# Performance work log

Measured on AMD Instinct MI355X. Metric: run time of the kernel, lower is better.

## Reference

```python
import jax, jax.numpy as jnp
import numpy as np
from jax import lax

B, T, EPROJS, DUNITS, ATT_DIM = 32, 2048, 1024, 1024, 512
ACONV_CHANS, ACONV_FILTS = 10, 100
KSIZE = 2 * ACONV_FILTS + 1  # 201
SCALING = 2.0


def setup_inputs() -> dict:
    key = jax.random.key(0)
    ks = jax.random.split(key, 16)
    lengths = jax.random.randint(ks[1], (B,), T // 2, T + 1, dtype=jnp.int32)
    # normalized uniform initial attention over valid frames (as in module's init branch)
    mask = jnp.arange(T)[None, :] < lengths[:, None]
    att_prev = mask.astype(jnp.float32) / lengths[:, None].astype(jnp.float32)
    s_e = 1.0 / np.sqrt(EPROJS)
    s_d = 1.0 / np.sqrt(DUNITS)
    s_a = 1.0 / np.sqrt(ATT_DIM)
    s_c = 1.0 / np.sqrt(ACONV_CHANS)
    return {
        "enc_hs_pad": jax.random.normal(ks[0], (B, T, EPROJS), jnp.float32),
        "enc_hs_len": lengths,
        "dec_z": jax.random.normal(ks[2], (B, DUNITS), jnp.float32),
        "att_prev": att_prev,
        "att_h": jax.random.normal(ks[3], (B, ATT_DIM), jnp.float32) * 0.1,
        "att_c": jax.random.normal(ks[4], (B, ATT_DIM), jnp.float32) * 0.1,
        "W_enc": jax.random.uniform(ks[5], (EPROJS, ATT_DIM), jnp.float32, -s_e, s_e),
        "b_enc": jax.random.uniform(ks[6], (ATT_DIM,), jnp.float32, -s_e, s_e),
        "W_dec": jax.random.uniform(ks[7], (DUNITS, ATT_DIM), jnp.float32, -s_d, s_d),
        "W_conv": jax.random.uniform(ks[8], (ACONV_CHANS, 1, KSIZE), jnp.float32, -0.1, 0.1),
        "W_ih": jax.random.uniform(ks[9], (4 * ATT_DIM, ACONV_CHANS), jnp.float32, -s_a, s_a),
        "W_hh": jax.random.uniform(ks[10], (4 * ATT_DIM, ATT_DIM), jnp.float32, -s_a, s_a),
        "W_g": jax.random.uniform(ks[11], (ATT_DIM, 1), jnp.float32, -s_a, s_a),
        "b_g": jax.random.uniform(ks[12], (1,), jnp.float32, -s_a, s_a),
    }


def reference(enc_hs_pad, enc_hs_len, dec_z, att_prev, att_h, att_c,
              W_enc, b_enc, W_dec, W_conv, W_ih, W_hh, W_g, b_g):
    # pre_compute_enc_h = mlp_enc(enc_h): (B, T, A)
    pre_enc = jnp.einsum("bte,ea->bta", enc_hs_pad, W_enc) + b_enc

    # location conv over previous attention: (B,1,T) -> (B,C,T)
    conv = lax.conv_general_dilated(
        att_prev[:, None, :], W_conv,
        window_strides=(1,), padding=[(ACONV_FILTS, ACONV_FILTS)],
        dimension_numbers=("NCH", "OIH", "NCH"))
    # relu + global max-pool over T -> (B, C)
    conv_feat = jnp.max(jax.nn.relu(conv), axis=2)

    # LSTMCell (no bias), PyTorch gate order i, f, g, o
    gates = conv_feat @ W_ih.T + att_h @ W_hh.T  # (B, 4A)
    i, f, g, o = jnp.split(gates, 4, axis=1)
    c_new = jax.nn.sigmoid(f) * att_c + jax.nn.sigmoid(i) * jnp.tanh(g)
    h_new = jax.nn.sigmoid(o) * jnp.tanh(c_new)

    dec_t = dec_z @ W_dec  # (B, A)
    # scoring: gvec(tanh(att_h + pre_enc + dec)) -> (B, T)
    e = (jnp.tanh(h_new[:, None, :] + pre_enc + dec_t[:, None, :]) @ W_g)[..., 0] + b_g[0]

    pad_mask = jnp.arange(e.shape[1])[None, :] >= enc_hs_len[:, None]
    e = jnp.where(pad_mask, -jnp.inf, e)
    w = jax.nn.softmax(SCALING * e, axis=1)  # (B, T)

    c = jnp.einsum("bt,bte->be", w, enc_hs_pad)  # (B, EPROJS)
    return c, w, h_new, c_new
```

## Files before the change

kernel.cpp:

```cpp
#include <hip/hip_runtime.h>
#include <hip/hip_bf16.h>
#include <cstddef>

#define BB      32
#define TT_ALL  2048
#define EPROJS  1024
#define DUNITS  1024
#define ATT     512
#define CH      10
#define KS      201
#define FILT    100

#define OFF_C   0
#define OFF_W   (BB*EPROJS)
#define OFF_H   (OFF_W + BB*TT_ALL)
#define OFF_CN  (OFF_H + BB*ATT)

#define WS_CF    0
#define WS_V     512
#define WS_E     16896
#define WS_WF    82432
#define WS_WT    147968
#define WS_PART  (WS_WT + 262144)
#define WS_GP    (WS_PART + 262144)
#define WS_DP    (WS_GP + 131072)

typedef __attribute__((ext_vector_type(8))) short short8;
typedef __attribute__((ext_vector_type(4))) float f32x4;

__device__ __forceinline__ float sigm(float x) { return 1.f / (1.f + expf(-x)); }
__device__ __forceinline__ unsigned short f2bf(float f) {
  unsigned u = __float_as_uint(f);
  return (unsigned short)((u + 0x7FFFu + ((u >> 16) & 1u)) >> 16);
}
__device__ __forceinline__ ushort2 f2bf2(float a, float b) {
  __hip_bfloat162 h = __float22bfloat162_rn(float2{a, b});
  return *reinterpret_cast<ushort2*>(&h);
}

__global__ __launch_bounds__(256) void k_wprep(const float* __restrict__ W,
                                               unsigned short* __restrict__ WT) {
  const int et = blockIdx.x >> 4;
  const int at = blockIdx.x & 15;
  const int e0 = et * 32, a0 = at * 32;
  __shared__ float st[32][36];
  const int tid = threadIdx.x;
  {
    const int r = tid >> 3, q = tid & 7;
    const float4 v4 = *reinterpret_cast<const float4*>(&W[(size_t)(e0 + r) * ATT + a0 + q * 4]);
    st[r][q * 4 + 0] = v4.x; st[r][q * 4 + 1] = v4.y;
    st[r][q * 4 + 2] = v4.z; st[r][q * 4 + 3] = v4.w;
  }
  __syncthreads();
  {
    const int a = tid >> 3, q = tid & 7;
    ushort4 h;
    h.x = f2bf(st[q * 4 + 0][a]); h.y = f2bf(st[q * 4 + 1][a]);
    h.z = f2bf(st[q * 4 + 2][a]); h.w = f2bf(st[q * 4 + 3][a]);
    *reinterpret_cast<ushort4*>(&WT[(size_t)(a0 + a) * EPROJS + e0 + q * 4]) = h;
  }
}

__global__ __launch_bounds__(256) void k_conv(const float* __restrict__ att_prev,
                                              const float* __restrict__ W_conv,
                                              float* __restrict__ conv_feat) {
  const int b  = blockIdx.x / CH;
  const int ch = blockIdx.x % CH;
  __shared__ float sprev[TT_ALL + 2 * FILT];
  __shared__ float sw[KS];
  __shared__ float red[4];
  const int tid = threadIdx.x;
  for (int i = tid; i < TT_ALL + 2 * FILT; i += 256) {
    int t = i - FILT;
    sprev[i] = (t >= 0 && t < TT_ALL) ? att_prev[b * TT_ALL + t] : 0.f;
  }
  for (int i = tid; i < KS; i += 256) sw[i] = W_conv[ch * KS + i];
  __syncthreads();
  float m = 0.f;
  for (int t = tid; t < TT_ALL; t += 256) {
    float s = 0.f;
    for (int k = 0; k < KS; ++k) s = fmaf(sprev[t + k], sw[k], s);
    m = fmaxf(m, s);
  }
  for (int off = 32; off; off >>= 1) m = fmaxf(m, __shfl_xor(m, off, 64));
  if ((tid & 63) == 0) red[tid >> 6] = m;
  __syncthreads();
  if (tid == 0)
    conv_feat[b * CH + ch] = fmaxf(fmaxf(red[0], red[1]), fmaxf(red[2], red[3]));
}

__global__ __launch_bounds__(256) void k_gates(const float* __restrict__ att_h,
                                               const float* __restrict__ W_hh,
                                               float* __restrict__ gp) {
  const int jt = blockIdx.x >> 1;
  const int sp = blockIdx.x & 1;
  const int j0 = jt * 64;
  const int k0 = sp * 256;
  const int tid = threadIdx.x;
  const int al = tid & 63, bg = tid >> 6;
  __shared__ float sW[64][65];
  __shared__ float sH[32][64];
  float acc[8];
#pragma unroll
  for (int i = 0; i < 8; ++i) acc[i] = 0.f;
  for (int kc = 0; kc < 256; kc += 64) {
    __syncthreads();
#pragma unroll
    for (int i = 0; i < 4; ++i) {
      const int f = tid + i * 256;
      const int r = f >> 4, q = f & 15;
      const float4 w4 = *reinterpret_cast<const float4*>(
          &W_hh[(size_t)(j0 + r) * ATT + k0 + kc + q * 4]);
      sW[r][q * 4 + 0] = w4.x; sW[r][q * 4 + 1] = w4.y;
      sW[r][q * 4 + 2] = w4.z; sW[r][q * 4 + 3] = w4.w;
    }
#pragma unroll
    for (int i = 0; i < 2; ++i) {
      const int g = tid + i * 256;
      const int r = g >> 4, q = g & 15;
      *reinterpret_cast<float4*>(&sH[r][q * 4]) = *reinterpret_cast<const float4*>(
          &att_h[(size_t)r * ATT + k0 + kc + q * 4]);
    }
    __syncthreads();
#pragma unroll 16
    for (int k = 0; k < 64; ++k) {
      const float w = sW[al][k];
#pragma unroll
      for (int bb = 0; bb < 8; ++bb)
        acc[bb] = fmaf(w, sH[bg * 8 + bb][k], acc[bb]);
    }
  }
#pragma unroll
  for (int bb = 0; bb < 8; ++bb)
    gp[((size_t)(sp * 32 + bg * 8 + bb)) * (4 * ATT) + j0 + al] = acc[bb];
}

__global__ __launch_bounds__(256) void k_dec(const float* __restrict__ dec_z,
                                             const float* __restrict__ W_dec,
                                             float* __restrict__ dp) {
  const int at = blockIdx.x >> 1;
  const int sp = blockIdx.x & 1;
  const int a0 = at * 64;
  const int d0 = sp * 512;
  const int tid = threadIdx.x;
  const int al = tid & 63, bg = tid >> 6;
  __shared__ float sW[64][64];
  __shared__ float sZ[32][64];
  float acc[8];
#pragma unroll
  for (int i = 0; i < 8; ++i) acc[i] = 0.f;
  for (int dc = 0; dc < 512; dc += 64) {
    __syncthreads();
#pragma unroll
    for (int i = 0; i < 4; ++i) {
      const int f = tid + i * 256;
      const int r = f >> 4, q = f & 15;
      *reinterpret_cast<float4*>(&sW[r][q * 4]) = *reinterpret_cast<const float4*>(
          &W_dec[(size_t)(d0 + dc + r) * ATT + a0 + q * 4]);
    }
#pragma unroll
    for (int i = 0; i < 2; ++i) {
      const int g = tid + i * 256;
      const int r = g >> 4, q = g & 15;
      *reinterpret_cast<float4*>(&sZ[r][q * 4]) = *reinterpret_cast<const float4*>(
          &dec_z[(size_t)r * DUNITS + d0 + dc + q * 4]);
    }
    __syncthreads();
#pragma unroll 16
    for (int d = 0; d < 64; ++d) {
      const float w = sW[d][al];
#pragma unroll
      for (int bb = 0; bb < 8; ++bb)
        acc[bb] = fmaf(sZ[bg * 8 + bb][d], w, acc[bb]);
    }
  }
#pragma unroll
  for (int bb = 0; bb < 8; ++bb)
    dp[((size_t)(sp * 32 + bg * 8 + bb)) * ATT + a0 + al] = acc[bb];
}

__global__ __launch_bounds__(256) void k_lstm_v(const float* __restrict__ gp,
                                                const float* __restrict__ dp,
                                                const float* __restrict__ conv_feat,
                                                const float* __restrict__ W_ih,
                                                const float* __restrict__ att_c,
                                                float* __restrict__ v,
                                                float* __restrict__ out) {
  const int b = blockIdx.x, tid = threadIdx.x;
  __shared__ float scf[CH];
  if (tid < CH) scf[tid] = conv_feat[b * CH + tid];
  __syncthreads();
  for (int a = tid; a < ATT; a += 256) {
    float g4[4];
#pragma unroll
    for (int q = 0; q < 4; ++q) {
      const int j = q * ATT + a;
      float g = gp[(size_t)b * (4 * ATT) + j] + gp[(size_t)(32 + b) * (4 * ATT) + j];
#pragma unroll
      for (int c = 0; c < CH; ++c) g = fmaf(scf[c], W_ih[(size_t)j * CH + c], g);
      g4[q] = g;
    }
    const float ig = sigm(g4[0]);
    const float fg = sigm(g4[1]);
    const float gg = tanhf(g4[2]);
    const float og = sigm(g4[3]);
    const float cN = fg * att_c[b * ATT + a] + ig * gg;
    const float hN = og * tanhf(cN);
    out[OFF_H + b * ATT + a]  = hN;
    out[OFF_CN + b * ATT + a] = cN;
    v[b * ATT + a] = hN + dp[(size_t)b * ATT + a] + dp[(size_t)(32 + b) * ATT + a];
  }
}

#define MT2 128
__global__ __launch_bounds__(512) void k_score_mfma(const float* __restrict__ enc,
                                                    const unsigned short* __restrict__ WT,
                                                    const float* __restrict__ b_enc,
                                                    const float* __restrict__ W_g,
                                                    const float* __restrict__ b_g,
                                                    const float* __restrict__ v,
                                                    const int* __restrict__ lens,
                                                    float* __restrict__ e_out) {
  const int b  = blockIdx.x >> 4;
  const int t0 = (blockIdx.x & 15) * MT2;
  const int len = lens[b];
  if (t0 >= len) return;
  const int tid = threadIdx.x;
  const int lane = tid & 63, wid = tid >> 6;
  const int l15 = lane & 15, l4 = lane >> 4;
  const int wm = wid >> 2, wn = wid & 3;
  const int a0w = wn * 128;

  __shared__ unsigned short sA[128][40];
  __shared__ unsigned short sW[512][40];
  __shared__ float red[128][5];

  const size_t encBase = ((size_t)b * TT_ALL + t0) * EPROJS;

  const int cA0 = tid, cA1 = tid + 512;
  const int rA0 = cA0 >> 3, qA0 = cA0 & 7;
  const int rA1 = cA1 >> 3, qA1 = cA1 & 7;
  int rW[4], pW[4];
#pragma unroll
  for (int i = 0; i < 4; ++i) {
    const int c = tid + i * 512;
    rW[i] = c >> 2; pW[i] = c & 3;
  }

  float4 ar[2];
  short8 wr[4];
  ar[0] = *reinterpret_cast<const float4*>(&enc[encBase + (size_t)rA0 * EPROJS + qA0 * 4]);
  ar[1] = *reinterpret_cast<const float4*>(&enc[encBase + (size_t)rA1 * EPROJS + qA1 * 4]);
#pragma unroll
  for (int i = 0; i < 4; ++i)
    wr[i] = *reinterpret_cast<const short8*>(&WT[(size_t)rW[i] * EPROJS + pW[i] * 8]);

  f32x4 acc[4][8];
#pragma unroll
  for (int m = 0; m < 4; ++m)
#pragma unroll
    for (int n = 0; n < 8; ++n) acc[m][n] = (f32x4){0.f, 0.f, 0.f, 0.f};

  for (int kk = 0; kk < EPROJS; kk += 32) {
    {
      ushort2 h0 = f2bf2(ar[0].x, ar[0].y), h1 = f2bf2(ar[0].z, ar[0].w);
      ushort4 h; h.x = h0.x; h.y = h0.y; h.z = h1.x; h.w = h1.y;
      *reinterpret_cast<ushort4*>(&sA[rA0][qA0 * 4]) = h;
      h0 = f2bf2(ar[1].x, ar[1].y); h1 = f2bf2(ar[1].z, ar[1].w);
      h.x = h0.x; h.y = h0.y; h.z = h1.x; h.w = h1.y;
      *reinterpret_cast<ushort4*>(&sA[rA1][qA1 * 4]) = h;
    }
#pragma unroll
    for (int i = 0; i < 4; ++i)
      *reinterpret_cast<short8*>(&sW[rW[i]][pW[i] * 8]) = wr[i];
    __syncthreads();
    if (kk + 32 < EPROJS) {
      const int kn = kk + 32;
      ar[0] = *reinterpret_cast<const float4*>(&enc[encBase + (size_t)rA0 * EPROJS + kn + qA0 * 4]);
      ar[1] = *reinterpret_cast<const float4*>(&enc[encBase + (size_t)rA1 * EPROJS + kn + qA1 * 4]);
#pragma unroll
      for (int i = 0; i < 4; ++i)
        wr[i] = *reinterpret_cast<const short8*>(&WT[(size_t)rW[i] * EPROJS + kn + pW[i] * 8]);
    }
    short8 af[4];
#pragma unroll
    for (int m = 0; m < 4; ++m)
      af[m] = *reinterpret_cast<const short8*>(&sA[wm * 64 + 16 * m + l15][l4 * 8]);
#pragma unroll
    for (int n = 0; n < 8; ++n) {
      const short8 bfr = *reinterpret_cast<const short8*>(&sW[a0w + 16 * n + l15][l4 * 8]);
#pragma unroll
      for (int m = 0; m < 4; ++m)
        acc[m][n] = __builtin_amdgcn_mfma_f32_16x16x32_bf16(af[m], bfr, acc[m][n], 0, 0, 0);
    }
    __syncthreads();
  }

  float rp[4][4];
#pragma unroll
  for (int m = 0; m < 4; ++m)
#pragma unroll
    for (int j = 0; j < 4; ++j) rp[m][j] = 0.f;
#pragma unroll
  for (int n = 0; n < 8; ++n) {
    const int a = a0w + 16 * n + l15;
    const float va = v[b * ATT + a] + b_enc[a];
    const float wg = W_g[a];
#pragma unroll
    for (int m = 0; m < 4; ++m)
#pragma unroll
      for (int j = 0; j < 4; ++j) {
        const float x = acc[m][n][j] + va;
        const float th = 1.f - 2.f / (__expf(2.f * x) + 1.f);
        rp[m][j] = fmaf(th, wg, rp[m][j]);
      }
  }
#pragma unroll
  for (int m = 0; m < 4; ++m)
#pragma unroll
    for (int j = 0; j < 4; ++j) {
      float s = rp[m][j];
      s += __shfl_xor(s, 1, 64);
      s += __shfl_xor(s, 2, 64);
      s += __shfl_xor(s, 4, 64);
      s += __shfl_xor(s, 8, 64);
      rp[m][j] = s;
    }
  if (l15 == 0) {
#pragma unroll
    for (int m = 0; m < 4; ++m)
#pragma unroll
      for (int j = 0; j < 4; ++j)
        red[wm * 64 + m * 16 + l4 * 4 + j][wn] = rp[m][j];
  }
  __syncthreads();
  if (tid < MT2) {
    const float s = b_g[0] + red[tid][0] + red[tid][1] + red[tid][2] + red[tid][3];
    e_out[b * TT_ALL + t0 + tid] = s;
  }
}

__global__ __launch_bounds__(256) void k_softmax(const float* __restrict__ e,
                                                 const int* __restrict__ lens,
                                                 float* __restrict__ wf,
                                                 float* __restrict__ out) {
  const int b = blockIdx.x, tid = threadIdx.x, len = lens[b];
  __shared__ float sbuf[4];
  float vals[8];
  float m = -1e30f;
#pragma unroll
  for (int i = 0; i < 8; ++i) {
    const int t = tid + i * 256;
    const float x = (t < len) ? e[b * TT_ALL + t] : -1e30f;
    vals[i] = x;
    m = fmaxf(m, x);
  }
  for (int off = 32; off; off >>= 1) m = fmaxf(m, __shfl_xor(m, off, 64));
  if ((tid & 63) == 0) sbuf[tid >> 6] = m;
  __syncthreads();
  m = fmaxf(fmaxf(sbuf[0], sbuf[1]), fmaxf(sbuf[2], sbuf[3]));
  __syncthreads();
  float s = 0.f;
#pragma unroll
  for (int i = 0; i < 8; ++i) {
    const int t = tid + i * 256;
    const float p = (t < len) ? expf(2.f * (vals[i] - m)) : 0.f;
    vals[i] = p;
    s += p;
  }
  for (int off = 32; off; off >>= 1) s += __shfl_xor(s, off, 64);
  if ((tid & 63) == 0) sbuf[tid >> 6] = s;
  __syncthreads();
  s = sbuf[0] + sbuf[1] + sbuf[2] + sbuf[3];
  const float inv = 1.f / s;
#pragma unroll
  for (int i = 0; i < 8; ++i) {
    const int t = tid + i * 256;
    const float wv = vals[i] * inv;
    wf[b * TT_ALL + t] = wv;
    out[OFF_W + b * TT_ALL + t] = wv;
  }
}

__global__ __launch_bounds__(256) void k_ctx(const float* __restrict__ enc,
                                             const float* __restrict__ wf,
                                             const int* __restrict__ lens,
                                             float* __restrict__ part) {
  const int blk = blockIdx.x;
  const int b  = blk >> 5;
  const int et = (blk >> 3) & 3;
  const int tc = blk & 7;
  const int tid = threadIdx.x;
  const int e = et * 256 + tid;
  const int len = lens[b];
  const int tbeg = tc * 256;
  const int tend = min(tbeg + 256, len);
  float a0 = 0.f, a1 = 0.f;
  int t = tbeg;
  for (; t + 2 <= tend; t += 2) {
    a0 = fmaf(wf[b * TT_ALL + t + 0], enc[((size_t)b * TT_ALL + t + 0) * EPROJS + e], a0);
    a1 = fmaf(wf[b * TT_ALL + t + 1], enc[((size_t)b * TT_ALL + t + 1) * EPROJS + e], a1);
  }
  for (; t < tend; ++t)
    a0 = fmaf(wf[b * TT_ALL + t], enc[((size_t)b * TT_ALL + t) * EPROJS + e], a0);
  part[((size_t)b * 8 + tc) * EPROJS + e] = a0 + a1;
}

__global__ __launch_bounds__(256) void k_comb(const float* __restrict__ part,
                                              float* __restrict__ out) {
  const int b = blockIdx.x >> 2, et = blockIdx.x & 3;
  const int e = et * 256 + threadIdx.x;
  float s = 0.f;
#pragma unroll
  for (int tc = 0; tc < 8; ++tc) s += part[((size_t)b * 8 + tc) * EPROJS + e];
  out[OFF_C + b * EPROJS + e] = s;
}

extern "C" void kernel_launch(void* const* d_in, const int* in_sizes, int n_in,
                              void* d_out, int out_size, void* d_ws, size_t ws_size,
                              hipStream_t stream) {
  const float* enc      = (const float*)d_in[0];
  const int*   lens     = (const int*)d_in[1];
  const float* dec_z    = (const float*)d_in[2];
  const float* att_prev = (const float*)d_in[3];
  const float* att_h    = (const float*)d_in[4];
  const float* att_c    = (const float*)d_in[5];
  const float* W_enc    = (const float*)d_in[6];
  const float* b_enc    = (const float*)d_in[7];
  const float* W_dec    = (const float*)d_in[8];
  const float* W_conv   = (const float*)d_in[9];
  const float* W_ih     = (const float*)d_in[10];
  const float* W_hh     = (const float*)d_in[11];
  const float* W_g      = (const float*)d_in[12];
  const float* b_g      = (const float*)d_in[13];
  float* out = (float*)d_out;
  float* ws  = (float*)d_ws;

  float* cf   = ws + WS_CF;
  float* v    = ws + WS_V;
  float* e_s  = ws + WS_E;
  float* wf   = ws + WS_WF;
  unsigned short* wt = (unsigned short*)(ws + WS_WT);
  float* part = ws + WS_PART;
  float* gp   = ws + WS_GP;
  float* dp   = ws + WS_DP;

  k_wprep     <<<512, 256, 0, stream>>>(W_enc, wt);
  k_conv      <<<BB * CH, 256, 0, stream>>>(att_prev, W_conv, cf);
  k_gates     <<<64, 256, 0, stream>>>(att_h, W_hh, gp);
  k_dec       <<<16, 256, 0, stream>>>(dec_z, W_dec, dp);
  k_lstm_v    <<<BB, 256, 0, stream>>>(gp, dp, cf, W_ih, att_c, v, out);
  k_score_mfma<<<BB * (TT_ALL / MT2), 512, 0, stream>>>(enc, wt, b_enc, W_g, b_g, v, lens, e_s);
  k_softmax   <<<BB, 256, 0, stream>>>(e_s, lens, wf, out);
  k_ctx       <<<BB * 32, 256, 0, stream>>>(enc, wf, lens, part);
  k_comb      <<<BB * 4, 256, 0, stream>>>(part, out);
}
```

Measured before the change: 236.8 us.

## Load MFMA fragments directly from global memory, dropping LDS staging and barriers

Result: slower. 376.6 us (+59.0%).

```diff
diff --git a/kernel.cpp b/kernel.cpp
--- a/kernel.cpp
+++ b/kernel.cpp
@@ -36,6 +36,12 @@
 __device__ __forceinline__ ushort2 f2bf2(float a, float b) {
   __hip_bfloat162 h = __float22bfloat162_rn(float2{a, b});
   return *reinterpret_cast<ushort2*>(&h);
+}
+__device__ __forceinline__ short8 pack_bf16x8(const float4 a, const float4 b) {
+  union { short8 s; ushort2 u[4]; } r;
+  r.u[0] = f2bf2(a.x, a.y); r.u[1] = f2bf2(a.z, a.w);
+  r.u[2] = f2bf2(b.x, b.y); r.u[3] = f2bf2(b.z, b.w);
+  return r.s;
 }
 
 __global__ __launch_bounds__(256) void k_wprep(const float* __restrict__ W,
@@ -213,14 +219,14 @@
 }
 
 #define MT2 128
-__global__ __launch_bounds__(512) void k_score_mfma(const float* __restrict__ enc,
-                                                    const unsigned short* __restrict__ WT,
-                                                    const float* __restrict__ b_enc,
-                                                    const float* __restrict__ W_g,
-                                                    const float* __restrict__ b_g,
-                                                    const float* __restrict__ v,
-                                                    const int* __restrict__ lens,
-                                                    float* __restrict__ e_out) {
+__global__ __launch_bounds__(512, 2) void k_score_mfma(const float* __restrict__ enc,
+                                                       const unsigned short* __restrict__ WT,
+                                                       const float* __restrict__ b_enc,
+                                                       const float* __restrict__ W_g,
+                                                       const float* __restrict__ b_g,
+                                                       const float* __restrict__ v,
+                                                       const int* __restrict__ lens,
+                                                       float* __restrict__ e_out) {
   const int b  = blockIdx.x >> 4;
   const int t0 = (blockIdx.x & 15) * MT2;
   const int len = lens[b];
@@ -231,29 +237,10 @@
   const int wm = wid >> 2, wn = wid & 3;
   const int a0w = wn * 128;
 
-  __shared__ unsigned short sA[128][40];
-  __shared__ unsigned short sW[512][40];
   __shared__ float red[128][5];
 
-  const size_t encBase = ((size_t)b * TT_ALL + t0) * EPROJS;
-
-  const int cA0 = tid, cA1 = tid + 512;
-  const int rA0 = cA0 >> 3, qA0 = cA0 & 7;
-  const int rA1 = cA1 >> 3, qA1 = cA1 & 7;
-  int rW[4], pW[4];
-#pragma unroll
-  for (int i = 0; i < 4; ++i) {
-    const int c = tid + i * 512;
-    rW[i] = c >> 2; pW[i] = c & 3;
-  }
-
-  float4 ar[2];
-  short8 wr[4];
-  ar[0] = *reinterpret_cast<const float4*>(&enc[encBase + (size_t)rA0 * EPROJS + qA0 * 4]);
-  ar[1] = *reinterpret_cast<const float4*>(&enc[encBase + (size_t)rA1 * EPROJS + qA1 * 4]);
-#pragma unroll
-  for (int i = 0; i < 4; ++i)
-    wr[i] = *reinterpret_cast<const short8*>(&WT[(size_t)rW[i] * EPROJS + pW[i] * 8]);
+  const float* pA = enc + ((size_t)b * TT_ALL + t0 + wm * 64 + l15) * EPROJS + l4 * 8;
+  const unsigned short* pB = WT + (size_t)(a0w + l15) * EPROJS + l4 * 8;
 
   f32x4 acc[4][8];
 #pragma unroll
@@ -262,38 +249,25 @@
     for (int n = 0; n < 8; ++n) acc[m][n] = (f32x4){0.f, 0.f, 0.f, 0.f};
 
   for (int kk = 0; kk < EPROJS; kk += 32) {
-    {
-      ushort2 h0 = f2bf2(ar[0].x, ar[0].y), h1 = f2bf2(ar[0].z, ar[0].w);
-      ushort4 h; h.x = h0.x; h.y = h0.y; h.z = h1.x; h.w = h1.y;
-      *reinterpret_cast<ushort4*>(&sA[rA0][qA0 * 4]) = h;
-      h0 = f2bf2(ar[1].x, ar[1].y); h1 = f2bf2(ar[1].z, ar[1].w);
-      h.x = h0.x; h.y = h0.y; h.z = h1.x; h.w = h1.y;
-      *reinterpret_cast<ushort4*>(&sA[rA1][qA1 * 4]) = h;
-    }
-#pragma unroll
-    for (int i = 0; i < 4; ++i)
-      *reinterpret_cast<short8*>(&sW[rW[i]][pW[i] * 8]) = wr[i];
-    __syncthreads();
-    if (kk + 32 < EPROJS) {
-      const int kn = kk + 32;
-      ar[0] = *reinterpret_cast<const float4*>(&enc[encBase + (size_t)rA0 * EPROJS + kn + qA0 * 4]);
-      ar[1] = *reinterpret_cast<const float4*>(&enc[encBase + (size_t)rA1 * EPROJS + kn + qA1 * 4]);
-#pragma unroll
-      for (int i = 0; i < 4; ++i)
-        wr[i] = *reinterpret_cast<const short8*>(&WT[(size_t)rW[i] * EPROJS + kn + pW[i] * 8]);
-    }
+    float4 a0[4], a1[4];
+#pragma unroll
+    for (int m = 0; m < 4; ++m) {
+      const float* p = pA + (size_t)m * 16 * EPROJS + kk;
+      a0[m] = *reinterpret_cast<const float4*>(p);
+      a1[m] = *reinterpret_cast<const float4*>(p + 4);
+    }
+    short8 bfr[8];
+#pragma unroll
+    for (int n = 0; n < 8; ++n)
+      bfr[n] = *reinterpret_cast<const short8*>(pB + (size_t)n * 16 * EPROJS + kk);
     short8 af[4];
 #pragma unroll
-    for (int m = 0; m < 4; ++m)
-      af[m] = *reinterpret_cast<const short8*>(&sA[wm * 64 + 16 * m + l15][l4 * 8]);
-#pragma unroll
-    for (int n = 0; n < 8; ++n) {
-      const short8 bfr = *reinterpret_cast<const short8*>(&sW[a0w + 16 * n + l15][l4 * 8]);
+    for (int m = 0; m < 4; ++m) af[m] = pack_bf16x8(a0[m], a1[m]);
+#pragma unroll
+    for (int n = 0; n < 8; ++n)
 #pragma unroll
       for (int m = 0; m < 4; ++m)
-        acc[m][n] = __builtin_amdgcn_mfma_f32_16x16x32_bf16(af[m], bfr, acc[m][n], 0, 0, 0);
-    }
-    __syncthreads();
+        acc[m][n] = __builtin_amdgcn_mfma_f32_16x16x32_bf16(af[m], bfr[n], acc[m][n], 0, 0, 0);
   }
 
   float rp[4][4];
```
